# Performance work log

Measured on AMD Instinct MI355X. Metric: run time of the kernel, lower is better.

The kernel has to match this reference:

```python
import jax, jax.numpy as jnp
import numpy as np

B = 4096          # batch_size
D = 256           # embedding dim
N = 2 * B
TEMPERATURE = 0.5
GAMMA = 2.0
ALPHA = 0.25


def _negative_indices():
    # Static column indices of negatives per row: all columns except self (i)
    # and the positive partner ((i+B) mod N). Shape (N, N-2).
    idx = []
    for i in range(N):
        partner = (i + B) % N
        cols = [j for j in range(N) if j != i and j != partner]
        idx.append(cols)
    return np.asarray(idx, dtype=np.int32)

_NEG_IDX = jnp.asarray(_negative_indices())


def setup_inputs() -> dict:
    key = jax.random.key(0)
    kx, ky = jax.random.split(key)
    zx = jax.random.normal(kx, (B, D), dtype=jnp.float32)
    zy = jax.random.normal(ky, (B, D), dtype=jnp.float32)
    return {"zx": zx, "zy": zy}


def reference(zx, zy):
    z = jnp.concatenate([zx, zy], axis=0)                    # (N, D)
    zn = z / jnp.linalg.norm(z, axis=1, keepdims=True)       # cosine normalize
    sim = (zn @ zn.T) / TEMPERATURE                          # (N, N)

    sim_xy = jnp.diagonal(sim, offset=B)                     # (B,)
    sim_yx = jnp.diagonal(sim, offset=-B)                    # (B,)
    pos = jnp.concatenate([sim_xy, sim_yx])[:, None]         # (N, 1)
    neg = jnp.take_along_axis(sim, _NEG_IDX, axis=1)         # (N, N-2)

    logits = jnp.concatenate([pos, neg], axis=1)             # (N, N-1)
    # CE with label 0 for every row: -log_softmax(logits)[:, 0]
    ce = jax.nn.logsumexp(logits, axis=1) - logits[:, 0]
    pt = jnp.exp(-ce)
    focal = (1.0 - pt) ** GAMMA * ce
    return (ALPHA * focal).mean()
```

## Files before the change

kernel.cpp:

```cpp
#include <hip/hip_runtime.h>
#include <stdint.h>
#include <stddef.h>


typedef __attribute__((ext_vector_type(8))) short short8;
typedef __attribute__((ext_vector_type(4))) float f32x4;

#define NROWS 8192
#define DDIM 256
#define NTILES 2080
#define NBLK 1040

__device__ __forceinline__ unsigned short f2bf(float f) {
  unsigned int u = __float_as_uint(f);
  u = (u + 0x7FFFu + ((u >> 16) & 1u)) >> 16;
  return (unsigned short)u;
}

__device__ __forceinline__ void unrank_tile(int t, int& p_out, int& q_out) {
  int p = (int)((129.0f - sqrtf((float)(16641 - 8 * t))) * 0.5f);
  p = max(0, min(63, p));
  while ((((p + 1) * (129 - (p + 1))) >> 1) <= t) ++p;
  while (((p * (129 - p)) >> 1) > t) --p;
  p_out = p;
  q_out = p + (t - ((p * (129 - p)) >> 1));
}

__global__ __launch_bounds__(256) void norm_kernel(const float* __restrict__ zx,
                                                   const float* __restrict__ zy,
                                                   unsigned short* __restrict__ zn,
                                                   unsigned int* __restrict__ counter) {
  if (blockIdx.x == 0 && threadIdx.x == 0) *counter = 0u;
  const int row = blockIdx.x * 4 + (threadIdx.x >> 6);
  const int lane = threadIdx.x & 63;
  const float* src = (row < 4096) ? (zx + (size_t)row * DDIM)
                                  : (zy + (size_t)(row - 4096) * DDIM);
  float4 v = reinterpret_cast<const float4*>(src)[lane];
  float ss = v.x * v.x + v.y * v.y + v.z * v.z + v.w * v.w;
#pragma unroll
  for (int m = 1; m < 64; m <<= 1) ss += __shfl_xor(ss, m);
  const float sc = 1.69864360f * rsqrtf(ss);
  ushort4 o;
  o.x = f2bf(v.x * sc); o.y = f2bf(v.y * sc);
  o.z = f2bf(v.z * sc); o.w = f2bf(v.w * sc);
  reinterpret_cast<ushort4*>(zn + (size_t)row * DDIM)[lane] = o;
}

__global__ __launch_bounds__(256, 4) void simtri_kernel(const unsigned short* __restrict__ zn,
                                                        float* __restrict__ partial,
                                                        float* __restrict__ pos) {
  __shared__ unsigned short smem[2][2][128 * 32];
  const int c = (blockIdx.x & 7) * 130 + (blockIdx.x >> 3);

  const int tid = threadIdx.x;
  const int lane = tid & 63;
  const int wid = tid >> 6;
  const int wr = wid >> 1;
  const int wc = wid & 1;
  const int hi = lane >> 4, lo = lane & 15;
  const int sw = lo & 3;

  const f32x4 z4 = {0.f, 0.f, 0.f, 0.f};
  f32x4 acc[4][4];
#pragma unroll
  for (int m = 0; m < 4; ++m)
#pragma unroll
    for (int n = 0; n < 4; ++n) acc[m][n] = z4;

  auto stage_one = [&](int buf, int which, int row0, int k0) {
    unsigned short* lb = &smem[buf][which][0];
#pragma unroll
    for (int j = 0; j < 2; ++j) {
      const int u = j * 256 + tid;
      const int r = u >> 2, ul = u & 3;
      const unsigned short* g =
          zn + (size_t)(row0 + r) * DDIM + k0 + ((ul ^ (r & 3)) << 3);
      unsigned short* l = lb + (size_t)(j * 256 + wid * 64) * 8;
      __builtin_amdgcn_global_load_lds(
          (const __attribute__((address_space(1))) void*)g,
          (__attribute__((address_space(3))) void*)l, 16, 0, 0);
    }
  };
  auto stageT = [&](int buf, int p, int q, int k0) {
    stage_one(buf, 0, p << 7, k0);
    if (p != q) stage_one(buf, 1, q << 7, k0);
  };

  int cp, cq;
  unrank_tile(2 * c, cp, cq);
  stageT(0, cp, cq, 0);
  __syncthreads();

  int buf = 0;
  for (int i = 0; i < 2; ++i) {
    int np = cp, nq = cq;
    const bool have_next = (i == 0);
    if (have_next) { if (cq == 63) { np = cp + 1; nq = np; } else { nq = cq + 1; } }
    const bool isdiag = (cp == cq);
    const bool ispos = (cq == cp + 32);
    const int R0 = cp << 7;
    const int C0 = cq << 7;

#pragma unroll
    for (int kk = 0; kk < 8; ++kk) {
      if (kk < 7) stageT(buf ^ 1, cp, cq, (kk + 1) * 32);
      else if (have_next) stageT(buf ^ 1, np, nq, 0);
      const unsigned short* A = &smem[buf][0][0];
      const unsigned short* Bm = isdiag ? A : &smem[buf][1][0];
      short8 af[4], bfr[4];
#pragma unroll
      for (int m = 0; m < 4; ++m)
        af[m] = *reinterpret_cast<const short8*>(
            A + ((wr * 64 + m * 16 + lo) * 32 + ((hi ^ sw) << 3)));
#pragma unroll
      for (int n = 0; n < 4; ++n)
        bfr[n] = *reinterpret_cast<const short8*>(
            Bm + ((wc * 64 + n * 16 + lo) * 32 + ((hi ^ sw) << 3)));
#pragma unroll
      for (int m = 0; m < 4; ++m)
#pragma unroll
        for (int n = 0; n < 4; ++n)
          acc[m][n] = __builtin_amdgcn_mfma_f32_16x16x32_bf16(af[m], bfr[n], acc[m][n], 0, 0, 0);
      buf ^= 1;
      if (kk < 7) __syncthreads();
    }

    float rsum[4][4];
    float csum[4];
#pragma unroll
    for (int m = 0; m < 4; ++m)
#pragma unroll
      for (int r = 0; r < 4; ++r) rsum[m][r] = 0.f;
#pragma unroll
    for (int n = 0; n < 4; ++n) csum[n] = 0.f;

#pragma unroll
    for (int m = 0; m < 4; ++m)
#pragma unroll
      for (int n = 0; n < 4; ++n)
#pragma unroll
        for (int r = 0; r < 4; ++r) {
          const float e = __builtin_amdgcn_exp2f(acc[m][n][r]);
          rsum[m][r] += e;
          csum[n] += e;
        }

    if ((isdiag || ispos) && (wr == wc)) {
#pragma unroll
      for (int m = 0; m < 4; ++m)
#pragma unroll
        for (int r = 0; r < 4; ++r)
          if (lo == 4 * hi + r) {
            if (isdiag) rsum[m][r] -= __builtin_amdgcn_exp2f(acc[m][m][r]);
            else        pos[R0 + wr * 64 + m * 16 + lo] = acc[m][m][r];
          }
    }

#pragma unroll
    for (int m = 0; m < 4; ++m)
#pragma unroll
      for (int r = 0; r < 4; ++r) {
        float s = rsum[m][r];
        s += __shfl_xor(s, 1); s += __shfl_xor(s, 2);
        s += __shfl_xor(s, 4); s += __shfl_xor(s, 8);
        if (lo == 0) {
          const int grow = R0 + wr * 64 + m * 16 + (hi << 2) + r;
          partial[(size_t)(cq * 2 + wc) * NROWS + grow] = s;
        }
      }

    if (!isdiag) {
#pragma unroll
      for (int n = 0; n < 4; ++n) {
        float cs = csum[n];
        cs += __shfl_xor(cs, 16); cs += __shfl_xor(cs, 32);
        if (lane < 16)
          partial[(size_t)(cp * 2 + wr) * NROWS + (C0 + wc * 64 + n * 16 + lane)] = cs;
      }
    }

#pragma unroll
    for (int m = 0; m < 4; ++m)
#pragma unroll
      for (int n = 0; n < 4; ++n) acc[m][n] = z4;

    __syncthreads();
    cp = np; cq = nq;
  }
}

__global__ __launch_bounds__(256) void d1_kernel(const float* __restrict__ partial,
                                                 const float* __restrict__ pos,
                                                 float* __restrict__ bsum,
                                                 float* __restrict__ out,
                                                 unsigned int* __restrict__ counter) {
  const int row = blockIdx.x * 256 + threadIdx.x;
  float s = 0.f;
#pragma unroll 16
  for (int c = 0; c < 128; ++c) s += partial[(size_t)c * NROWS + row];
  const float L = __log2f(s) - pos[row & 4095];
  const float pt = __builtin_amdgcn_exp2f(-L);
  const float ce = 0.69314718056f * L;
  float f = (1.f - pt) * (1.f - pt) * ce;
#pragma unroll
  for (int m = 1; m < 64; m <<= 1) f += __shfl_xor(f, m);
  __shared__ float wsum[4];
  if ((threadIdx.x & 63) == 0) wsum[threadIdx.x >> 6] = f;
  __syncthreads();
  if (threadIdx.x == 0) {
    bsum[blockIdx.x] = wsum[0] + wsum[1] + wsum[2] + wsum[3];
    __threadfence();
    if (atomicAdd(counter, 1u) == 31u) {
      __threadfence();
      float v = 0.f;
#pragma unroll
      for (int c = 0; c < 32; ++c) v += ((const volatile float*)bsum)[c];
      out[0] = 0.25f * v / 8192.f;
    }
  }
}

extern "C" void kernel_launch(void* const* d_in, const int* in_sizes, int n_in,
                              void* d_out, int out_size, void* d_ws, size_t ws_size,
                              hipStream_t stream) {
  const float* zx = (const float*)d_in[0];
  const float* zy = (const float*)d_in[1];
  float* out = (float*)d_out;

  unsigned short* zn = (unsigned short*)d_ws;
  float* pos = (float*)((char*)d_ws + (size_t)NROWS * DDIM * 2);
  float* partial = pos + 4096;
  float* bsum = partial + (size_t)128 * NROWS;
  unsigned int* counter = (unsigned int*)(bsum + 32);

  norm_kernel<<<2048, 256, 0, stream>>>(zx, zy, zn, counter);
  simtri_kernel<<<NBLK, 256, 0, stream>>>(zn, partial, pos);
  d1_kernel<<<32, 256, 0, stream>>>(partial, pos, bsum, out, counter);
}
```

Before: 116.8 us.

## Use persistent blocks with a triple-buffered async load pipeline in simtri

Drops the grid from 1040 to 512 blocks, with each block walking a contiguous run of 4 or 5 triangular tiles. K-slices are streamed through a three-stage LDS ring using explicit vmcnt waits and raw barriers, so global-to-LDS loads stay in flight across tile boundaries and tile epilogues. The aim is to hide load latency and cut per-block setup and barrier cost. In exchange, occupancy drops (launch bounds 2, more shared memory), the 5-tile blocks create load imbalance, and diagonal tiles now load their B operand redundantly.

```diff
diff --git a/kernel.cpp b/kernel.cpp
--- a/kernel.cpp
+++ b/kernel.cpp
@@ -9,7 +9,7 @@
 #define NROWS 8192
 #define DDIM 256
 #define NTILES 2080
-#define NBLK 1040
+#define NBLK 512
 
 __device__ __forceinline__ unsigned short f2bf(float f) {
   unsigned int u = __float_as_uint(f);
@@ -46,11 +46,15 @@
   reinterpret_cast<ushort4*>(zn + (size_t)row * DDIM)[lane] = o;
 }
 
-__global__ __launch_bounds__(256, 4) void simtri_kernel(const unsigned short* __restrict__ zn,
+__global__ __launch_bounds__(256, 2) void simtri_kernel(const unsigned short* __restrict__ zn,
                                                         float* __restrict__ partial,
                                                         float* __restrict__ pos) {
-  __shared__ unsigned short smem[2][2][128 * 32];
-  const int c = (blockIdx.x & 7) * 130 + (blockIdx.x >> 3);
+  __shared__ unsigned short smem[3][2][128 * 32];
+  const int c = (blockIdx.x & 7) * 64 + (blockIdx.x >> 3);
+  int start, nt;
+  if (c < 32) { start = c * 5;              nt = 5; }
+  else        { start = 160 + (c - 32) * 4; nt = 4; }
+  const int NS = nt * 8;
 
   const int tid = threadIdx.x;
   const int lane = tid & 63;
@@ -67,64 +71,53 @@
 #pragma unroll
     for (int n = 0; n < 4; ++n) acc[m][n] = z4;
 
-  auto stage_one = [&](int buf, int which, int row0, int k0) {
-    unsigned short* lb = &smem[buf][which][0];
-#pragma unroll
-    for (int j = 0; j < 2; ++j) {
-      const int u = j * 256 + tid;
-      const int r = u >> 2, ul = u & 3;
-      const unsigned short* g =
-          zn + (size_t)(row0 + r) * DDIM + k0 + ((ul ^ (r & 3)) << 3);
-      unsigned short* l = lb + (size_t)(j * 256 + wid * 64) * 8;
-      __builtin_amdgcn_global_load_lds(
-          (const __attribute__((address_space(1))) void*)g,
-          (__attribute__((address_space(3))) void*)l, 16, 0, 0);
-    }
-  };
-  auto stageT = [&](int buf, int p, int q, int k0) {
-    stage_one(buf, 0, p << 7, k0);
-    if (p != q) stage_one(buf, 1, q << 7, k0);
-  };
-
-  int cp, cq;
-  unrank_tile(2 * c, cp, cq);
-  stageT(0, cp, cq, 0);
-  __syncthreads();
-
-  int buf = 0;
-  for (int i = 0; i < 2; ++i) {
-    int np = cp, nq = cq;
-    const bool have_next = (i == 0);
-    if (have_next) { if (cq == 63) { np = cp + 1; nq = np; } else { nq = cq + 1; } }
+  auto stage_pair = [&](int b, int p, int q, int k0) {
+#pragma unroll
+    for (int which = 0; which < 2; ++which) {
+      const int row0 = (which ? q : p) << 7;
+      unsigned short* lb = &smem[b][which][0];
+#pragma unroll
+      for (int j = 0; j < 2; ++j) {
+        const int u = j * 256 + tid;
+        const int r = u >> 2, ul = u & 3;
+        const unsigned short* g =
+            zn + (size_t)(row0 + r) * DDIM + k0 + ((ul ^ (r & 3)) << 3);
+        unsigned short* l = lb + (size_t)(j * 256 + wid * 64) * 8;
+        __builtin_amdgcn_global_load_lds(
+            (const __attribute__((address_space(1))) void*)g,
+            (__attribute__((address_space(3))) void*)l, 16, 0, 0);
+      }
+    }
+  };
+
+  auto consume = [&](int b) {
+    const unsigned short* A = &smem[b][0][0];
+    const unsigned short* Bm = &smem[b][1][0];
+    short8 af[4], bfr[4];
+#pragma unroll
+    for (int m = 0; m < 4; ++m)
+      af[m] = *reinterpret_cast<const short8*>(
+          A + ((wr * 64 + m * 16 + lo) * 32 + ((hi ^ sw) << 3)));
+#pragma unroll
+    for (int n = 0; n < 4; ++n)
+      bfr[n] = *reinterpret_cast<const short8*>(
+          Bm + ((wc * 64 + n * 16 + lo) * 32 + ((hi ^ sw) << 3)));
+#pragma unroll
+    for (int m = 0; m < 4; ++m)
+#pragma unroll
+      for (int n = 0; n < 4; ++n)
+        acc[m][n] = __builtin_amdgcn_mfma_f32_16x16x32_bf16(af[m], bfr[n], acc[m][n], 0, 0, 0);
+  };
+
+  auto advance = [&](int& p, int& q) {
+    if (q == 63) { ++p; q = p; } else { ++q; }
+  };
+
+  auto epilogue = [&](int cp, int cq) {
     const bool isdiag = (cp == cq);
     const bool ispos = (cq == cp + 32);
     const int R0 = cp << 7;
     const int C0 = cq << 7;
-
-#pragma unroll
-    for (int kk = 0; kk < 8; ++kk) {
-      if (kk < 7) stageT(buf ^ 1, cp, cq, (kk + 1) * 32);
-      else if (have_next) stageT(buf ^ 1, np, nq, 0);
-      const unsigned short* A = &smem[buf][0][0];
-      const unsigned short* Bm = isdiag ? A : &smem[buf][1][0];
-      short8 af[4], bfr[4];
-#pragma unroll
-      for (int m = 0; m < 4; ++m)
-        af[m] = *reinterpret_cast<const short8*>(
-            A + ((wr * 64 + m * 16 + lo) * 32 + ((hi ^ sw) << 3)));
-#pragma unroll
-      for (int n = 0; n < 4; ++n)
-        bfr[n] = *reinterpret_cast<const short8*>(
-            Bm + ((wc * 64 + n * 16 + lo) * 32 + ((hi ^ sw) << 3)));
-#pragma unroll
-      for (int m = 0; m < 4; ++m)
-#pragma unroll
-        for (int n = 0; n < 4; ++n)
-          acc[m][n] = __builtin_amdgcn_mfma_f32_16x16x32_bf16(af[m], bfr[n], acc[m][n], 0, 0, 0);
-      buf ^= 1;
-      if (kk < 7) __syncthreads();
-    }
-
     float rsum[4][4];
     float csum[4];
 #pragma unroll
@@ -133,7 +126,6 @@
       for (int r = 0; r < 4; ++r) rsum[m][r] = 0.f;
 #pragma unroll
     for (int n = 0; n < 4; ++n) csum[n] = 0.f;
-
 #pragma unroll
     for (int m = 0; m < 4; ++m)
 #pragma unroll
@@ -144,7 +136,6 @@
           rsum[m][r] += e;
           csum[n] += e;
         }
-
     if ((isdiag || ispos) && (wr == wc)) {
 #pragma unroll
       for (int m = 0; m < 4; ++m)
@@ -155,7 +146,6 @@
             else        pos[R0 + wr * 64 + m * 16 + lo] = acc[m][m][r];
           }
     }
-
 #pragma unroll
     for (int m = 0; m < 4; ++m)
 #pragma unroll
@@ -168,7 +158,6 @@
           partial[(size_t)(cq * 2 + wc) * NROWS + grow] = s;
         }
       }
-
     if (!isdiag) {
 #pragma unroll
       for (int n = 0; n < 4; ++n) {
@@ -178,15 +167,47 @@
           partial[(size_t)(cp * 2 + wr) * NROWS + (C0 + wc * 64 + n * 16 + lane)] = cs;
       }
     }
-
-#pragma unroll
-    for (int m = 0; m < 4; ++m)
-#pragma unroll
-      for (int n = 0; n < 4; ++n) acc[m][n] = z4;
-
-    __syncthreads();
-    cp = np; cq = nq;
+  };
+
+  int cp, cq;
+  unrank_tile(start, cp, cq);
+  int sp = cp, sq = cq;
+  stage_pair(0, sp, sq, 0);
+  stage_pair(1, sp, sq, 32);
+  stage_pair(2, sp, sq, 64);
+
+  int bsel = 0;
+  for (int k = 0; k < NS - 2; ++k) {
+    asm volatile("s_waitcnt vmcnt(8)" ::: "memory");
+    __builtin_amdgcn_s_barrier();
+    __builtin_amdgcn_sched_barrier(0);
+    consume(bsel);
+    if ((k & 7) == 7) {
+      epilogue(cp, cq);
+      advance(cp, cq);
+#pragma unroll
+      for (int m = 0; m < 4; ++m)
+#pragma unroll
+        for (int n = 0; n < 4; ++n) acc[m][n] = z4;
+    }
+    __builtin_amdgcn_s_barrier();
+    const int t = k + 3;
+    if (t < NS) {
+      if ((t & 7) == 0) advance(sp, sq);
+      stage_pair(bsel, sp, sq, (t & 7) * 32);
+    }
+    bsel = (bsel == 2) ? 0 : bsel + 1;
   }
+  asm volatile("s_waitcnt vmcnt(4)" ::: "memory");
+  __builtin_amdgcn_s_barrier();
+  __builtin_amdgcn_sched_barrier(0);
+  consume(bsel);
+  bsel = (bsel == 2) ? 0 : bsel + 1;
+  asm volatile("s_waitcnt vmcnt(0)" ::: "memory");
+  __builtin_amdgcn_s_barrier();
+  __builtin_amdgcn_sched_barrier(0);
+  consume(bsel);
+  epilogue(cp, cq);
 }
 
 __global__ __launch_bounds__(256) void d1_kernel(const float* __restrict__ partial,
```

Result: faster. 111.5 us (-4.5%).
